# Optimization experiments

Hardware: AMD Instinct MI355X
Metric: run time of the kernel (lower is better)

## Reference

```python
import jax, jax.numpy as jnp
import numpy as np

D_IN = 128
D = 128
B, N = 2, 512
EPS = 1e-5


def _glorot(key, shape):
    fan_in = shape[-1]
    bound = 1.0 / np.sqrt(fan_in)
    return jax.random.uniform(key, shape, jnp.float32, -bound, bound)


def setup_inputs() -> dict:
    key = jax.random.key(0)
    ks = jax.random.split(key, 20)
    x = jax.random.normal(ks[0], (B, N, D_IN), jnp.float32)
    adj = jax.random.uniform(ks[1], (B, N, N), jnp.float32)
    return {
        "x": x,
        "adj": adj,
        # input linear
        "W_lin": _glorot(ks[2], (D, D_IN)), "b_lin": _glorot(ks[3], (D,)),
        # message network: Linear(D+1,D) -> ReLU -> Linear(D,D)
        "W_m1": _glorot(ks[4], (D, D + 1)), "b_m1": _glorot(ks[5], (D,)),
        "W_m2": _glorot(ks[6], (D, D)), "b_m2": _glorot(ks[7], (D,)),
        # DenseAtt: Linear(2D+1, 1) -> sigmoid
        "W_att": _glorot(ks[8], (1, 2 * D + 1)), "b_att": _glorot(ks[9], (1,)),
        # output network: Linear(D,D) -> ReLU -> Linear(D,D)
        "W_o1": _glorot(ks[10], (D, D)), "b_o1": _glorot(ks[11], (D,)),
        "W_o2": _glorot(ks[12], (D, D)), "b_o2": _glorot(ks[13], (D,)),
        # layernorm
        "ln_g": jnp.ones((D,), jnp.float32), "ln_b": jnp.zeros((D,), jnp.float32),
    }


def reference(x, adj, W_lin, b_lin, W_m1, b_m1, W_m2, b_m2,
              W_att, b_att, W_o1, b_o1, W_o2, b_o2, ln_g, ln_b):
    # input transform: [B,N,D]
    h = jnp.einsum('bnd,od->bno', x, W_lin) + b_lin
    b, n, d = h.shape
    adj_e = adj[..., None]                               # [B,N,N,1]
    h_right = jnp.broadcast_to(h[:, None, :, :], (b, n, n, d))  # neighbor features
    h_left = jnp.broadcast_to(h[:, :, None, :], (b, n, n, d))   # center features

    # message network on concat(h_right, adj): [B,N,N,D+1] -> [B,N,N,D]
    msg_in = jnp.concatenate([h_right, adj_e], axis=-1)
    m = jax.nn.relu(jnp.einsum('bnme,oe->bnmo', msg_in, W_m1) + b_m1)
    m = jnp.einsum('bnmd,od->bnmo', m, W_m2) + b_m2

    # dense attention: sigmoid(Linear(concat(h_left, h_right, adj)))
    att_in = jnp.concatenate([h_left, h_right, adj_e], axis=-1)  # [B,N,N,2D+1]
    att = jax.nn.sigmoid(jnp.einsum('bnme,oe->bnmo', att_in, W_att) + b_att)  # [B,N,N,1]

    # attention-weighted sum over neighbors (dim=2)
    agg = jnp.sum(m * att, axis=2)                       # [B,N,D]

    # output network
    agg = jax.nn.relu(jnp.einsum('bnd,od->bno', agg, W_o1) + b_o1)
    agg = jnp.einsum('bnd,od->bno', agg, W_o2) + b_o2

    u = h + agg
    # layernorm over last dim
    mu = jnp.mean(u, axis=-1, keepdims=True)
    var = jnp.mean(jnp.square(u - mu), axis=-1, keepdims=True)
    u = (u - mu) * jax.lax.rsqrt(var + EPS) * ln_g + ln_b
    out = jax.nn.relu(u)
    return out, adj
```

## Files before the change

kernel.cpp:

```cpp
#include <hip/hip_runtime.h>
#include <hip/hip_bf16.h>
#include <math.h>

#define NN 512
#define DD 128
#define ROWS 1024
#define NR 4

__device__ __forceinline__ float sigmoidf_(float z){ return 1.0f/(1.0f + __expf(-z)); }

__global__ __launch_bounds__(512) void k_rows(
    const float* __restrict__ x, const float* __restrict__ W_lin, const float* __restrict__ b_lin,
    const float* __restrict__ W_m1, const float* __restrict__ b_m1,
    const float* __restrict__ W_att,
    const float* __restrict__ W_m2, const float* __restrict__ W_o1, const float* __restrict__ W_o2,
    float* __restrict__ h, __hip_bfloat16* __restrict__ hm1b,
    float* __restrict__ dotL, float* __restrict__ dotR,
    float* __restrict__ Wt_m2, float* __restrict__ Wt_o1, float* __restrict__ Wt_o2)
{
    const int r0   = blockIdx.x * NR;
    const int t    = threadIdx.x;
    const int rr   = t >> 7;
    const int o    = t & 127;
    const int q    = t >> 7;
    const int g    = t >> 6;
    const int lane = t & 63;

    __shared__ float xs[NR][DD];
    __shared__ float hs[NR][DD];
    __shared__ float pb2[4][NR][DD];

    ((float*)xs)[t] = x[r0 * DD + t];
    __syncthreads();

    {
        float a[NR] = {0.f, 0.f, 0.f, 0.f};
        const float4* wp = (const float4*)(W_lin + o * DD + q * 32);
        #pragma unroll
        for (int k = 0; k < 8; k++) {
            float4 w4 = wp[k];
            int d = q * 32 + 4 * k;
            #pragma unroll
            for (int r = 0; r < NR; r++) {
                float4 xv = *(const float4*)&xs[r][d];
                a[r] = fmaf(xv.x, w4.x, a[r]);
                a[r] = fmaf(xv.y, w4.y, a[r]);
                a[r] = fmaf(xv.z, w4.z, a[r]);
                a[r] = fmaf(xv.w, w4.w, a[r]);
            }
        }
        #pragma unroll
        for (int r = 0; r < NR; r++) pb2[q][r][o] = a[r];
    }
    __syncthreads();
    {
        float hreg = b_lin[o] + pb2[0][rr][o] + pb2[1][rr][o]
                              + pb2[2][rr][o] + pb2[3][rr][o];
        hs[rr][o] = hreg;
        h[(r0 + rr) * DD + o] = hreg;
    }
    __syncthreads();

    {
        int row = g & 3;
        const float* wa = W_att + (g >> 2) * DD;
        float p = hs[row][lane] * wa[lane] + hs[row][lane + 64] * wa[lane + 64];
        #pragma unroll
        for (int off = 32; off >= 1; off >>= 1) p += __shfl_down(p, off, 64);
        if (lane == 0) {
            if (g < 4) dotL[r0 + row] = p;
            else       dotR[r0 + row] = p;
        }
    }

    {
        float a[NR] = {0.f, 0.f, 0.f, 0.f};
        const float* w2 = W_m1 + o * (DD + 1) + q * 32;
        #pragma unroll
        for (int k = 0; k < 8; k++) {
            int d = q * 32 + 4 * k;
            float w0 = w2[4*k], w1 = w2[4*k+1], w2v = w2[4*k+2], w3 = w2[4*k+3];
            #pragma unroll
            for (int r = 0; r < NR; r++) {
                float4 xv = *(const float4*)&hs[r][d];
                a[r] = fmaf(xv.x, w0,  a[r]);
                a[r] = fmaf(xv.y, w1,  a[r]);
                a[r] = fmaf(xv.z, w2v, a[r]);
                a[r] = fmaf(xv.w, w3,  a[r]);
            }
        }
        #pragma unroll
        for (int r = 0; r < NR; r++) pb2[q][r][o] = a[r];
    }
    __syncthreads();
    {
        float v = b_m1[o] + pb2[0][rr][o] + pb2[1][rr][o]
                          + pb2[2][rr][o] + pb2[3][rr][o];
        hm1b[(r0 + rr) * DD + o] = __float2bfloat16(v);
    }

    if (blockIdx.x < 48 && t < 128) {
        const int w = blockIdx.x >> 4;
        const int s = blockIdx.x & 15;
        const float* src = (w == 0) ? W_m2 : (w == 1) ? W_o1 : W_o2;
        float*       dst = (w == 0) ? Wt_m2 : (w == 1) ? Wt_o1 : Wt_o2;
        #pragma unroll
        for (int j = 0; j < 8; j++)
            dst[t * DD + s * 8 + j] = src[(s * 8 + j) * DD + t];
    }
}

__global__ __launch_bounds__(512) void k_msgout(
    const float* __restrict__ adj, const unsigned int* __restrict__ hm1u,
    const float* __restrict__ dotL, const float* __restrict__ dotR,
    const float* __restrict__ W_m1, const float* __restrict__ W_att, const float* __restrict__ b_att,
    const float* __restrict__ Wt_m2, const float* __restrict__ b_m2,
    const float* __restrict__ Wt_o1, const float* __restrict__ b_o1,
    const float* __restrict__ Wt_o2, const float* __restrict__ b_o2,
    const float* __restrict__ h, const float* __restrict__ ln_g, const float* __restrict__ ln_b,
    float* __restrict__ out, float* __restrict__ out_adj)
{
    const int r0   = blockIdx.x * NR;
    const int b    = r0 >> 9;
    const int t    = threadIdx.x;
    const int g    = t >> 6;
    const int lane = t & 63;
    const int rr   = t >> 7;
    const int o    = t & 127;
    const int oq   = t & 31;
    const int dg   = t >> 5;

    __shared__ float2 aa[NR][NN];
    __shared__ float2 red[8][NR][64];
    __shared__ float  pb[4][4][16][32];
    __shared__ float  vs[NR][DD];
    __shared__ float  vs2[NR][DD];
    __shared__ float2 wa1s[64];
    __shared__ float  satt[NR];
    __shared__ float  redsc[2][2][NR];

    if (t < 64)
        wa1s[t] = make_float2(W_m1[(2 * t) * (DD + 1) + DD],
                              W_m1[(2 * t + 1) * (DD + 1) + DD]);
    const float wAdj = W_att[2 * DD];
    const float bA   = b_att[0];

    {
        float drm = dotR[b * NN + t];
        #pragma unroll
        for (int i = 0; i < NR; i++) {
            float a = adj[(r0 + i) * NN + t];
            out_adj[(r0 + i) * NN + t] = a;
            float z = dotL[r0 + i] + drm + a * wAdj + bA;
            aa[i][t] = make_float2(a, sigmoidf_(z));
        }
    }
    __syncthreads();

    if (g < NR) {
        float s = 0.f;
        #pragma unroll
        for (int k = 0; k < 8; k++) s += aa[g][lane + 64 * k].y;
        #pragma unroll
        for (int off = 32; off >= 1; off >>= 1) s += __shfl_down(s, off, 64);
        if (lane == 0) satt[g] = s;
    }

    {
        float2 agg[NR];
        #pragma unroll
        for (int r = 0; r < NR; r++) agg[r] = make_float2(0.f, 0.f);
        float2 wa = wa1s[lane];
        const unsigned int* hbase = hm1u + (size_t)b * NN * 64 + lane;
        #pragma unroll 4
        for (int m = g; m < NN; m += 8) {
            unsigned int u = hbase[m * 64];
            float2 hv;
            hv.x = __uint_as_float(u << 16);
            hv.y = __uint_as_float(u & 0xffff0000u);
            #pragma unroll
            for (int r = 0; r < NR; r++) {
                float2 at = aa[r][m];
                float u0 = fmaxf(fmaf(at.x, wa.x, hv.x), 0.f);
                float u1 = fmaxf(fmaf(at.x, wa.y, hv.y), 0.f);
                agg[r].x = fmaf(at.y, u0, agg[r].x);
                agg[r].y = fmaf(at.y, u1, agg[r].y);
            }
        }
        #pragma unroll
        for (int r = 0; r < NR; r++) red[g][r][lane] = agg[r];
    }
    __syncthreads();
    {
        float s = 0.f;
        #pragma unroll
        for (int gg = 0; gg < 8; gg++)
            s += ((const float*)&red[gg][rr][0])[o];
        vs[rr][o] = s;
    }
    __syncthreads();

    {
        float a0[4], a1[4], a2[4], a3[4];
        #pragma unroll
        for (int r = 0; r < 4; r++) { a0[r]=0.f; a1[r]=0.f; a2[r]=0.f; a3[r]=0.f; }
        #pragma unroll
        for (int k = 0; k < 8; k++) {
            int d = dg * 8 + k;
            float4 w4 = *(const float4*)(Wt_m2 + d * DD + oq * 4);
            #pragma unroll
            for (int r = 0; r < 4; r++) {
                float xv = vs[r][d];
                a0[r] = fmaf(w4.x, xv, a0[r]);
                a1[r] = fmaf(w4.y, xv, a1[r]);
                a2[r] = fmaf(w4.z, xv, a2[r]);
                a3[r] = fmaf(w4.w, xv, a3[r]);
            }
        }
        #pragma unroll
        for (int r = 0; r < 4; r++) {
            pb[0][r][dg][oq] = a0[r]; pb[1][r][dg][oq] = a1[r];
            pb[2][r][dg][oq] = a2[r]; pb[3][r][dg][oq] = a3[r];
        }
    }
    __syncthreads();
    {
        float s = 0.f;
        #pragma unroll
        for (int d16 = 0; d16 < 16; d16++) s += pb[o & 3][rr][d16][o >> 2];
        vs2[rr][o] = s + b_m2[o] * satt[rr];
    }
    __syncthreads();

    {
        float a0[4], a1[4], a2[4], a3[4];
        #pragma unroll
        for (int r = 0; r < 4; r++) { a0[r]=0.f; a1[r]=0.f; a2[r]=0.f; a3[r]=0.f; }
        #pragma unroll
        for (int k = 0; k < 8; k++) {
            int d = dg * 8 + k;
            float4 w4 = *(const float4*)(Wt_o1 + d * DD + oq * 4);
            #pragma unroll
            for (int r = 0; r < 4; r++) {
                float xv = vs2[r][d];
                a0[r] = fmaf(w4.x, xv, a0[r]);
                a1[r] = fmaf(w4.y, xv, a1[r]);
                a2[r] = fmaf(w4.z, xv, a2[r]);
                a3[r] = fmaf(w4.w, xv, a3[r]);
            }
        }
        #pragma unroll
        for (int r = 0; r < 4; r++) {
            pb[0][r][dg][oq] = a0[r]; pb[1][r][dg][oq] = a1[r];
            pb[2][r][dg][oq] = a2[r]; pb[3][r][dg][oq] = a3[r];
        }
    }
    __syncthreads();
    {
        float s = 0.f;
        #pragma unroll
        for (int d16 = 0; d16 < 16; d16++) s += pb[o & 3][rr][d16][o >> 2];
        vs[rr][o] = fmaxf(s + b_o1[o], 0.f);
    }
    __syncthreads();

    {
        float a0[4], a1[4], a2[4], a3[4];
        #pragma unroll
        for (int r = 0; r < 4; r++) { a0[r]=0.f; a1[r]=0.f; a2[r]=0.f; a3[r]=0.f; }
        #pragma unroll
        for (int k = 0; k < 8; k++) {
            int d = dg * 8 + k;
            float4 w4 = *(const float4*)(Wt_o2 + d * DD + oq * 4);
            #pragma unroll
            for (int r = 0; r < 4; r++) {
                float xv = vs[r][d];
                a0[r] = fmaf(w4.x, xv, a0[r]);
                a1[r] = fmaf(w4.y, xv, a1[r]);
                a2[r] = fmaf(w4.z, xv, a2[r]);
                a3[r] = fmaf(w4.w, xv, a3[r]);
            }
        }
        #pragma unroll
        for (int r = 0; r < 4; r++) {
            pb[0][r][dg][oq] = a0[r]; pb[1][r][dg][oq] = a1[r];
            pb[2][r][dg][oq] = a2[r]; pb[3][r][dg][oq] = a3[r];
        }
    }
    __syncthreads();

    float v;
    {
        float s = 0.f;
        #pragma unroll
        for (int d16 = 0; d16 < 16; d16++) s += pb[o & 3][rr][d16][o >> 2];
        v = s + b_o2[o] + h[(r0 + rr) * DD + o];
    }

    {
        float p1 = v, p2 = v * v;
        #pragma unroll
        for (int off = 32; off >= 1; off >>= 1) {
            p1 += __shfl_down(p1, off, 64);
            p2 += __shfl_down(p2, off, 64);
        }
        int wid = (t >> 6) & 1;
        if ((t & 63) == 0) { redsc[wid][0][rr] = p1; redsc[wid][1][rr] = p2; }
    }
    __syncthreads();
    {
        float sum = redsc[0][0][rr] + redsc[1][0][rr];
        float sq  = redsc[0][1][rr] + redsc[1][1][rr];
        float mu  = sum * (1.0f / DD);
        float var = sq * (1.0f / DD) - mu * mu;
        float inv = rsqrtf(var + 1e-5f);
        out[(r0 + rr) * DD + o] = fmaxf(fmaf((v - mu) * inv, ln_g[o], ln_b[o]), 0.f);
    }
}

extern "C" void kernel_launch(void* const* d_in, const int* in_sizes, int n_in,
                              void* d_out, int out_size, void* d_ws, size_t ws_size,
                              hipStream_t stream)
{
    (void)in_sizes; (void)n_in; (void)out_size; (void)ws_size;
    const float* x     = (const float*)d_in[0];
    const float* adj   = (const float*)d_in[1];
    const float* W_lin = (const float*)d_in[2];
    const float* b_lin = (const float*)d_in[3];
    const float* W_m1  = (const float*)d_in[4];
    const float* b_m1  = (const float*)d_in[5];
    const float* W_m2  = (const float*)d_in[6];
    const float* b_m2  = (const float*)d_in[7];
    const float* W_att = (const float*)d_in[8];
    const float* b_att = (const float*)d_in[9];
    const float* W_o1  = (const float*)d_in[10];
    const float* b_o1  = (const float*)d_in[11];
    const float* W_o2  = (const float*)d_in[12];
    const float* b_o2  = (const float*)d_in[13];
    const float* ln_g  = (const float*)d_in[14];
    const float* ln_b  = (const float*)d_in[15];

    float* out     = (float*)d_out;
    float* out_adj = out + ROWS * DD;

    float* ws    = (float*)d_ws;
    float* hm1   = ws;
    float* dotL  = ws + 131072;
    float* dotR  = ws + 132096;
    float* h     = ws + 133120;
    float* Wt_m2 = ws + 264192;
    float* Wt_o1 = ws + 280576;
    float* Wt_o2 = ws + 296960;

    hipLaunchKernelGGL(k_rows, dim3(ROWS / NR), dim3(512), 0, stream,
                       x, W_lin, b_lin, W_m1, b_m1, W_att, W_m2, W_o1, W_o2,
                       h, (__hip_bfloat16*)hm1, dotL, dotR, Wt_m2, Wt_o1, Wt_o2);
    hipLaunchKernelGGL(k_msgout, dim3(ROWS / NR), dim3(512), 0, stream,
                       adj, (const unsigned int*)hm1, dotL, dotR, W_m1, W_att, b_att,
                       Wt_m2, b_m2, Wt_o1, b_o1, Wt_o2, b_o2,
                       h, ln_g, ln_b, out, out_adj);
}
```

Measured before the change: 26.67 us.

## Store transposed weights in bf16, prefetch into registers, pack aggregation math

The three transposed output-network weight matrices are now stored as bf16 instead of fp32, which halves their global traffic. Each thread loads its slice of all three matrices into registers at kernel start, so the loads overlap the adjacency and aggregation phases instead of stalling the later matvecs. The inner aggregation loop is rewritten with 2-wide vector FMA and max builtins so the compiler can emit packed fp32 instructions. The cost is reduced weight precision and higher register pressure from 48 extra prefetched registers.

```diff
diff --git a/kernel.cpp b/kernel.cpp
--- a/kernel.cpp
+++ b/kernel.cpp
@@ -7,7 +7,18 @@
 #define ROWS 1024
 #define NR 4
 
+typedef float f32x2 __attribute__((ext_vector_type(2)));
+
 __device__ __forceinline__ float sigmoidf_(float z){ return 1.0f/(1.0f + __expf(-z)); }
+
+__device__ __forceinline__ float4 bf4(uint2 u) {
+    float4 w;
+    w.x = __uint_as_float(u.x << 16);
+    w.y = __uint_as_float(u.x & 0xffff0000u);
+    w.z = __uint_as_float(u.y << 16);
+    w.w = __uint_as_float(u.y & 0xffff0000u);
+    return w;
+}
 
 __global__ __launch_bounds__(512) void k_rows(
     const float* __restrict__ x, const float* __restrict__ W_lin, const float* __restrict__ b_lin,
@@ -16,7 +27,8 @@
     const float* __restrict__ W_m2, const float* __restrict__ W_o1, const float* __restrict__ W_o2,
     float* __restrict__ h, __hip_bfloat16* __restrict__ hm1b,
     float* __restrict__ dotL, float* __restrict__ dotR,
-    float* __restrict__ Wt_m2, float* __restrict__ Wt_o1, float* __restrict__ Wt_o2)
+    __hip_bfloat16* __restrict__ Wt_m2, __hip_bfloat16* __restrict__ Wt_o1,
+    __hip_bfloat16* __restrict__ Wt_o2)
 {
     const int r0   = blockIdx.x * NR;
     const int t    = threadIdx.x;
@@ -103,10 +115,10 @@
         const int w = blockIdx.x >> 4;
         const int s = blockIdx.x & 15;
         const float* src = (w == 0) ? W_m2 : (w == 1) ? W_o1 : W_o2;
-        float*       dst = (w == 0) ? Wt_m2 : (w == 1) ? Wt_o1 : Wt_o2;
+        __hip_bfloat16* dst = (w == 0) ? Wt_m2 : (w == 1) ? Wt_o1 : Wt_o2;
         #pragma unroll
         for (int j = 0; j < 8; j++)
-            dst[t * DD + s * 8 + j] = src[(s * 8 + j) * DD + t];
+            dst[t * DD + s * 8 + j] = __float2bfloat16(src[(s * 8 + j) * DD + t]);
     }
 }
 
@@ -114,9 +126,9 @@
     const float* __restrict__ adj, const unsigned int* __restrict__ hm1u,
     const float* __restrict__ dotL, const float* __restrict__ dotR,
     const float* __restrict__ W_m1, const float* __restrict__ W_att, const float* __restrict__ b_att,
-    const float* __restrict__ Wt_m2, const float* __restrict__ b_m2,
-    const float* __restrict__ Wt_o1, const float* __restrict__ b_o1,
-    const float* __restrict__ Wt_o2, const float* __restrict__ b_o2,
+    const __hip_bfloat16* __restrict__ Wt_m2, const float* __restrict__ b_m2,
+    const __hip_bfloat16* __restrict__ Wt_o1, const float* __restrict__ b_o1,
+    const __hip_bfloat16* __restrict__ Wt_o2, const float* __restrict__ b_o2,
     const float* __restrict__ h, const float* __restrict__ ln_g, const float* __restrict__ ln_b,
     float* __restrict__ out, float* __restrict__ out_adj)
 {
@@ -139,6 +151,20 @@
     __shared__ float  satt[NR];
     __shared__ float  redsc[2][2][NR];
 
+    uint2 pre1[8], pre2[8], pre3[8];
+    {
+        const unsigned short* w1 = (const unsigned short*)Wt_m2;
+        const unsigned short* w2 = (const unsigned short*)Wt_o1;
+        const unsigned short* w3 = (const unsigned short*)Wt_o2;
+        #pragma unroll
+        for (int k = 0; k < 8; k++) {
+            int off = (dg * 8 + k) * DD + oq * 4;
+            pre1[k] = *(const uint2*)(w1 + off);
+            pre2[k] = *(const uint2*)(w2 + off);
+            pre3[k] = *(const uint2*)(w3 + off);
+        }
+    }
+
     if (t < 64)
         wa1s[t] = make_float2(W_m1[(2 * t) * (DD + 1) + DD],
                               W_m1[(2 * t + 1) * (DD + 1) + DD]);
@@ -167,28 +193,31 @@
     }
 
     {
-        float2 agg[NR];
-        #pragma unroll
-        for (int r = 0; r < NR; r++) agg[r] = make_float2(0.f, 0.f);
-        float2 wa = wa1s[lane];
+        f32x2 agg[NR];
+        #pragma unroll
+        for (int r = 0; r < NR; r++) agg[r] = (f32x2){0.f, 0.f};
+        float2 wa0 = wa1s[lane];
+        f32x2 wav = {wa0.x, wa0.y};
+        const f32x2 zero2 = {0.f, 0.f};
         const unsigned int* hbase = hm1u + (size_t)b * NN * 64 + lane;
         #pragma unroll 4
         for (int m = g; m < NN; m += 8) {
             unsigned int u = hbase[m * 64];
-            float2 hv;
+            f32x2 hv;
             hv.x = __uint_as_float(u << 16);
             hv.y = __uint_as_float(u & 0xffff0000u);
             #pragma unroll
             for (int r = 0; r < NR; r++) {
                 float2 at = aa[r][m];
-                float u0 = fmaxf(fmaf(at.x, wa.x, hv.x), 0.f);
-                float u1 = fmaxf(fmaf(at.x, wa.y, hv.y), 0.f);
-                agg[r].x = fmaf(at.y, u0, agg[r].x);
-                agg[r].y = fmaf(at.y, u1, agg[r].y);
-            }
-        }
-        #pragma unroll
-        for (int r = 0; r < NR; r++) red[g][r][lane] = agg[r];
+                f32x2 adj2 = {at.x, at.x};
+                f32x2 att2 = {at.y, at.y};
+                f32x2 uu = __builtin_elementwise_fma(adj2, wav, hv);
+                uu = __builtin_elementwise_max(uu, zero2);
+                agg[r] = __builtin_elementwise_fma(att2, uu, agg[r]);
+            }
+        }
+        #pragma unroll
+        for (int r = 0; r < NR; r++) red[g][r][lane] = make_float2(agg[r].x, agg[r].y);
     }
     __syncthreads();
     {
@@ -207,7 +236,7 @@
         #pragma unroll
         for (int k = 0; k < 8; k++) {
             int d = dg * 8 + k;
-            float4 w4 = *(const float4*)(Wt_m2 + d * DD + oq * 4);
+            float4 w4 = bf4(pre1[k]);
             #pragma unroll
             for (int r = 0; r < 4; r++) {
                 float xv = vs[r][d];
@@ -239,7 +268,7 @@
         #pragma unroll
         for (int k = 0; k < 8; k++) {
             int d = dg * 8 + k;
-            float4 w4 = *(const float4*)(Wt_o1 + d * DD + oq * 4);
+            float4 w4 = bf4(pre2[k]);
             #pragma unroll
             for (int r = 0; r < 4; r++) {
                 float xv = vs2[r][d];
@@ -271,7 +300,7 @@
         #pragma unroll
         for (int k = 0; k < 8; k++) {
             int d = dg * 8 + k;
-            float4 w4 = *(const float4*)(Wt_o2 + d * DD + oq * 4);
+            float4 w4 = bf4(pre3[k]);
             #pragma unroll
             for (int r = 0; r < 4; r++) {
                 float xv = vs[r][d];
@@ -354,9 +383,12 @@
 
     hipLaunchKernelGGL(k_rows, dim3(ROWS / NR), dim3(512), 0, stream,
                        x, W_lin, b_lin, W_m1, b_m1, W_att, W_m2, W_o1, W_o2,
-                       h, (__hip_bfloat16*)hm1, dotL, dotR, Wt_m2, Wt_o1, Wt_o2);
+                       h, (__hip_bfloat16*)hm1, dotL, dotR,
+                       (__hip_bfloat16*)Wt_m2, (__hip_bfloat16*)Wt_o1, (__hip_bfloat16*)Wt_o2);
     hipLaunchKernelGGL(k_msgout, dim3(ROWS / NR), dim3(512), 0, stream,
                        adj, (const unsigned int*)hm1, dotL, dotR, W_m1, W_att, b_att,
-                       Wt_m2, b_m2, Wt_o1, b_o1, Wt_o2, b_o2,
+                       (const __hip_bfloat16*)Wt_m2, b_m2,
+                       (const __hip_bfloat16*)Wt_o1, b_o1,
+                       (const __hip_bfloat16*)Wt_o2, b_o2,
                        h, ln_g, ln_b, out, out_adj);
 }
```

Measured after the change: 40.36 us. 1.51x slower.
